# Optimization experiments

Hardware: AMD Instinct MI355X
Metric: run time of the kernel (lower is better)

Reference implementation:

```python
import jax, jax.numpy as jnp
import numpy as np

HEADS = 16
KV_HEADS = 8
HEAD_DIM = 128
HIDDEN = 2048
INTER = 8192
NUM_STATES = 4
WINDOW = 4096
EPS = 1e-6
THETA = 10000.0


def rms_norm(x, w):
    v = jnp.mean(jnp.square(x), axis=-1, keepdims=True)
    return x * jax.lax.rsqrt(v + EPS) * w


def rotate_half(x):
    h = x.shape[-1] // 2
    return jnp.concatenate((-x[..., h:], x[..., :h]), axis=-1)


def setup_inputs() -> dict:
    key = jax.random.key(0)
    ks = jax.random.split(key, 12)
    b, s = 1, 2048
    init = lambda k, shape: jax.random.normal(k, shape, jnp.float32) * 0.02
    return {
        "hidden_states": jax.random.normal(ks[0], (b, s, HIDDEN), jnp.float32),
        "sid": jax.random.randint(ks[1], (b, s), 0, NUM_STATES, dtype=jnp.int32),
        "position_ids": jnp.broadcast_to(jnp.arange(s, dtype=jnp.int32)[None, :], (b, s)),
        "ln1_w": jnp.ones((HIDDEN,), jnp.float32),
        "w_q": init(ks[2], (HEADS * HEAD_DIM, HIDDEN)),
        "w_k": init(ks[3], (KV_HEADS * HEAD_DIM, HIDDEN)),
        "w_v": init(ks[4], (KV_HEADS * HEAD_DIM, HIDDEN)),
        "w_o": init(ks[5], (HIDDEN, HEADS * HEAD_DIM)),
        "ln2_w": jnp.ones((HIDDEN,), jnp.float32),
        "w_gate": init(ks[6], (INTER, HIDDEN)),
        "w_up": init(ks[7], (INTER, HIDDEN)),
        "w_down": init(ks[8], (HIDDEN, INTER)),
    }


def reference(hidden_states, sid, position_ids, ln1_w, w_q, w_k, w_v, w_o, ln2_w, w_gate, w_up, w_down):
    b, s, _ = hidden_states.shape
    resid = hidden_states
    x = rms_norm(hidden_states, ln1_w)
    q = (x @ w_q.T).reshape(b, s, HEADS, HEAD_DIM).transpose(0, 2, 1, 3)      # [b,h,s,d]
    k = (x @ w_k.T).reshape(b, s, KV_HEADS, HEAD_DIM).transpose(0, 2, 1, 3)
    v = (x @ w_v.T).reshape(b, s, KV_HEADS, HEAD_DIM).transpose(0, 2, 1, 3)
    # RoPE (BoSsRotaryEmbedding + apply_rotary_pos_emb with unsqueeze_dim=1)
    inv_freq = 1.0 / (THETA ** (jnp.arange(0, HEAD_DIM, 2, dtype=jnp.float32) / HEAD_DIM))
    freqs = position_ids.astype(jnp.float32)[:, :, None] * inv_freq[None, None, :]  # [b,s,d/2]
    emb = jnp.concatenate((freqs, freqs), axis=-1)
    cos = jnp.cos(emb)[:, None]  # [b,1,s,d]
    sin = jnp.sin(emb)[:, None]
    q = q * cos + rotate_half(q) * sin
    k = k * cos + rotate_half(k) * sin
    # GQA: repeat_kv
    rep = HEADS // KV_HEADS
    k = jnp.repeat(k, rep, axis=1)
    v = jnp.repeat(v, rep, axis=1)
    # State-segment mask: stable sort by sid + causal varlen flash attention with
    # sliding window == dense attention masked to same-sid, causal, rank-window.
    same = sid[:, :, None] == sid[:, None, :]                                  # [b,s,s]
    causal = jnp.tril(jnp.ones((s, s), bool))
    tri = jnp.tril(jnp.ones((s, s), jnp.int32), -1)
    rank = jnp.einsum('bij,ij->bi', same.astype(jnp.int32), tri)               # within-segment position
    win = (rank[:, :, None] - rank[:, None, :]) <= WINDOW
    mask = same & causal[None] & win                                           # [b,s,s]
    scale = HEAD_DIM ** -0.5
    scores = jnp.einsum('bhqd,bhkd->bhqk', q, k) * scale
    scores = jnp.where(mask[:, None], scores, -jnp.inf)
    probs = jax.nn.softmax(scores, axis=-1)
    o = jnp.einsum('bhqk,bhkd->bhqd', probs, v)
    o = o.transpose(0, 2, 1, 3).reshape(b, s, HEADS * HEAD_DIM)
    h = resid + o @ w_o.T
    y = rms_norm(h, ln2_w)
    mlp = (jax.nn.silu(y @ w_gate.T) * (y @ w_up.T)) @ w_down.T
    return h + mlp
```

## Files before the change

### kernel.cpp

```cpp
#include <hip/hip_runtime.h>
#include <hip/hip_bf16.h>
#include <math.h>

#define SEQ    2048
#define HIDDEN 2048
#define INTER  8192
#define NHEADS 16
#define KVH    8
#define HD     128

typedef __bf16 bf16x8 __attribute__((ext_vector_type(8)));
typedef __bf16 bf16x4 __attribute__((ext_vector_type(4)));
typedef float  f32x4  __attribute__((ext_vector_type(4)));

typedef __attribute__((address_space(1))) void* as1v;
typedef __attribute__((address_space(3))) void* as3v;

__device__ __forceinline__ void g2l16(const void* g, void* l) {
    __builtin_amdgcn_global_load_lds((as1v)g, (as3v)l, 16, 0, 0);
}

#define OFF_WQ 0UL
#define OFF_WK 4194304UL
#define OFF_WV 6291456UL
#define OFF_WO 8388608UL
#define OFF_WG 12582912UL
#define OFF_WU 29360128UL
#define OFF_WD 46137344UL
#define W_TOTAL 62914560UL

__global__ __launch_bounds__(256) void k_cvt(
        const float* __restrict__ wq, const float* __restrict__ wk,
        const float* __restrict__ wv, const float* __restrict__ wo,
        const float* __restrict__ wg, const float* __restrict__ wu,
        const float* __restrict__ wd, __bf16* __restrict__ wb) {
    size_t e = ((size_t)blockIdx.x * 256 + threadIdx.x) * 8;
    const float* src; size_t base;
    if      (e < OFF_WK) { src = wq; base = OFF_WQ; }
    else if (e < OFF_WV) { src = wk; base = OFF_WK; }
    else if (e < OFF_WO) { src = wv; base = OFF_WV; }
    else if (e < OFF_WG) { src = wo; base = OFF_WO; }
    else if (e < OFF_WU) { src = wg; base = OFF_WG; }
    else if (e < OFF_WD) { src = wu; base = OFF_WU; }
    else                 { src = wd; base = OFF_WD; }
    const float4* s = (const float4*)(src + (e - base));
    float4 a = s[0], b = s[1];
    bf16x8 o;
    o[0] = (__bf16)a.x; o[1] = (__bf16)a.y; o[2] = (__bf16)a.z; o[3] = (__bf16)a.w;
    o[4] = (__bf16)b.x; o[5] = (__bf16)b.y; o[6] = (__bf16)b.z; o[7] = (__bf16)b.w;
    *(bf16x8*)(wb + e) = o;
}

__global__ __launch_bounds__(256) void k_rmsnorm(const float* __restrict__ x,
                                                 const float* __restrict__ w,
                                                 __bf16* __restrict__ out) {
    int row = blockIdx.x;
    int t   = threadIdx.x;
    const float4* xr = (const float4*)(x + (size_t)row * HIDDEN);
    float4 a = xr[t];
    float4 b = xr[t + 256];
    float ss = a.x*a.x + a.y*a.y + a.z*a.z + a.w*a.w
             + b.x*b.x + b.y*b.y + b.z*b.z + b.w*b.w;
#pragma unroll
    for (int d = 32; d > 0; d >>= 1) ss += __shfl_xor(ss, d);
    __shared__ float red[4];
    if ((t & 63) == 0) red[t >> 6] = ss;
    __syncthreads();
    float tot = red[0] + red[1] + red[2] + red[3];
    float r = rsqrtf(tot * (1.0f / (float)HIDDEN) + 1e-6f);
    const float4* wr = (const float4*)w;
    float4 wa = wr[t], wb = wr[t + 256];
    __bf16* o = out + (size_t)row * HIDDEN;
    bf16x4 pa, pb;
    pa[0] = (__bf16)(a.x * r * wa.x);
    pa[1] = (__bf16)(a.y * r * wa.y);
    pa[2] = (__bf16)(a.z * r * wa.z);
    pa[3] = (__bf16)(a.w * r * wa.w);
    pb[0] = (__bf16)(b.x * r * wb.x);
    pb[1] = (__bf16)(b.y * r * wb.y);
    pb[2] = (__bf16)(b.z * r * wb.z);
    pb[3] = (__bf16)(b.w * r * wb.w);
    *(bf16x4*)(o + 4*t)        = pa;
    *(bf16x4*)(o + 4*t + 1024) = pb;
}

__device__ __forceinline__ int gncol(int wn, int nt, int l15) {
    return wn*32 + ((nt & 1) << 4) + ((nt >> 1) << 6) + l15;
}

__device__ __forceinline__ void gemm_core(const __bf16* __restrict__ A, int lda,
                                          const __bf16* __restrict__ B, int ldb,
                                          int K, int m0, int n0,
                                          __bf16* As, __bf16* Bs,
                                          f32x4 acc[4][4]) {
    int tid  = threadIdx.x;
    int wave = tid >> 6;
    int lane = tid & 63;
    int quad = lane >> 4;
    int l15  = lane & 15;
    int wm = wave >> 1, wn = wave & 1;

    int srow = wave*32 + (lane >> 2);
    int scol = (lane & 3) * 8;
    char* adst = (char*)As + wave*2048 + lane*16;
    char* bdst = (char*)Bs + wave*2048 + lane*16;

    for (int k0 = 0; k0 < K; k0 += 32) {
        __syncthreads();
        g2l16(A + (size_t)(m0 + srow)      * lda + k0 + scol, adst);
        g2l16(A + (size_t)(m0 + srow + 16) * lda + k0 + scol, adst + 1024);
        g2l16(B + (size_t)(n0 + srow)      * ldb + k0 + scol, bdst);
        g2l16(B + (size_t)(n0 + srow + 16) * ldb + k0 + scol, bdst + 1024);
        __syncthreads();

        bf16x8 af[4], bfr[4];
#pragma unroll
        for (int mt = 0; mt < 4; ++mt)
            af[mt] = *(const bf16x8*)((const char*)As +
                        (wm*64 + mt*16 + l15)*64 + quad*16);
#pragma unroll
        for (int nt = 0; nt < 4; ++nt) {
            int r = gncol(wn, nt, l15);
            bfr[nt] = *(const bf16x8*)((const char*)Bs + r*64 + quad*16);
        }
#pragma unroll
        for (int mt = 0; mt < 4; ++mt)
#pragma unroll
            for (int nt = 0; nt < 4; ++nt)
                acc[mt][nt] = __builtin_amdgcn_mfma_f32_16x16x32_bf16(
                                  af[mt], bfr[nt], acc[mt][nt], 0, 0, 0);
    }
}

__device__ __forceinline__ void zero_acc(f32x4 acc[4][4]) {
#pragma unroll
    for (int i = 0; i < 4; ++i)
#pragma unroll
        for (int j = 0; j < 4; ++j) {
            acc[i][j][0] = 0.f; acc[i][j][1] = 0.f;
            acc[i][j][2] = 0.f; acc[i][j][3] = 0.f;
        }
}

#define MFMA_BF16 __builtin_amdgcn_mfma_f32_16x16x32_bf16
#define VMC asm volatile("s_waitcnt vmcnt(4)" ::: "memory")
#define NOSTMT ((void)0)

#define STAGE_A(BUF, HALF, TILE) do {                                         \
    const __bf16* _s = Aptr + (size_t)(m0 + (HALF)*128 + stgRow) * 2048       \
                      + ((size_t)(TILE) << 6) + stgCol;                       \
    char* _d = (char*)smem + (BUF)*65536 + (HALF)*16384 + stgDst;             \
    g2l16(_s, _d);                                                            \
    g2l16(_s + 8*2048, _d + 1024);                                            \
} while (0)

#define STAGE_B(BUF, HALF, TILE) do {                                         \
    const __bf16* _s = Bptr + (size_t)(n0 + (HALF)*128 + stgRow) * 2048       \
                      + ((size_t)(TILE) << 6) + stgCol;                       \
    char* _d = (char*)smem + (BUF)*65536 + 32768 + (HALF)*16384 + stgDst;     \
    g2l16(_s, _d);                                                            \
    g2l16(_s + 8*2048, _d + 1024);                                            \
} while (0)

#define PHASE(BUF, MH, NH, STAGE_STMT, VMWAIT) do {                           \
    bf16x8 _af[4][2], _bf[2][2];                                              \
    {                                                                         \
        const char* _Ab = (const char*)smem + (BUF)*65536 + (MH)*16384 + aRow;\
        const char* _Bb = (const char*)smem + (BUF)*65536 + 32768             \
                          + (NH)*16384 + bRow;                                \
        _Pragma("unroll")                                                     \
        for (int _m = 0; _m < 4; ++_m) {                                      \
            _af[_m][0] = *(const bf16x8*)(_Ab + _m*2048 + off0);              \
            _af[_m][1] = *(const bf16x8*)(_Ab + _m*2048 + (off0^64));         \
        }                                                                     \
        _Pragma("unroll")                                                     \
        for (int _n = 0; _n < 2; ++_n) {                                      \
            _bf[_n][0] = *(const bf16x8*)(_Bb + _n*2048 + off0);              \
            _bf[_n][1] = *(const bf16x8*)(_Bb + _n*2048 + (off0^64));         \
        }                                                                     \
    }                                                                         \
    STAGE_STMT;                                                               \
    VMWAIT;                                                                   \
    asm volatile("" ::: "memory");                                            \
    __builtin_amdgcn_s_barrier();                                             \
    asm volatile("" ::: "memory");                                            \
    __builtin_amdgcn_s_setprio(1);                                            \
    _Pragma("unroll")                                                         \
    for (int _m = 0; _m < 4; ++_m)                                            \
        _Pragma("unroll")                                                     \
        for (int _n = 0; _n < 2; ++_n) {                                      \
            acc[MH][NH][_m][_n] = MFMA_BF16(_af[_m][0], _bf[_n][0],           \
                                            acc[MH][NH][_m][_n], 0, 0, 0);    \
            acc[MH][NH][_m][_n] = MFMA_BF16(_af[_m][1], _bf[_n][1],           \
                                            acc[MH][NH][_m][_n], 0, 0, 0);    \
        }                                                                     \
    __builtin_amdgcn_s_setprio(0);                                            \
    asm volatile("" ::: "memory");                                            \
    __builtin_amdgcn_s_barrier();                                             \
    asm volatile("" ::: "memory");                                            \
} while (0)

__global__ __launch_bounds__(512, 2) void k_mlp256(
        const __bf16* __restrict__ Aptr,
        const __bf16* __restrict__ Bptr,
        __bf16* __restrict__ outb,
        int mode) {
    __shared__ char smem[131072];

    int flat = blockIdx.y * 32 + blockIdx.x;
    int swz  = (flat & 7) * 32 + (flat >> 3);
    int m0 = (swz >> 5) * 256;
    int n0 = (swz & 31) * 256;

    int tid  = threadIdx.x;
    int wave = tid >> 6, lane = tid & 63;
    int wm = wave >> 2, wn = wave & 3;
    int quad = lane >> 4, l15 = lane & 15;
    int cx   = l15 & 7;
    int off0 = (quad ^ cx) << 4;
    int aRow = (wm*64 + l15) << 7;
    int bRow = (wn*32 + l15) << 7;
    int stgRow = wave*16 + (lane >> 3);
    int stgCol = ((lane & 7) ^ (lane >> 3)) << 3;
    int stgDst = wave*2048 + lane*16;

    f32x4 acc[2][2][4][2];
#pragma unroll
    for (int a = 0; a < 2; ++a)
#pragma unroll
        for (int b = 0; b < 2; ++b)
#pragma unroll
            for (int c = 0; c < 4; ++c)
#pragma unroll
                for (int d = 0; d < 2; ++d) {
                    acc[a][b][c][d][0] = 0.f; acc[a][b][c][d][1] = 0.f;
                    acc[a][b][c][d][2] = 0.f; acc[a][b][c][d][3] = 0.f;
                }

    STAGE_A(0, 0, 0); STAGE_B(0, 0, 0);
    STAGE_A(0, 1, 0); STAGE_B(0, 1, 0);
    STAGE_A(1, 0, 1); STAGE_B(1, 0, 1);
    VMC;
    asm volatile("" ::: "memory");
    __builtin_amdgcn_s_barrier();
    asm volatile("" ::: "memory");

    const int NT = 32, TM = 31;
    for (int i = 0; i < NT/2; ++i) {
        int t1 = (2*i + 1) & TM;
        int t2 = (2*i + 2) & TM;
        int t3 = (2*i + 3) & TM;
        PHASE(0, 0, 0, STAGE_A(1, 1, t1), NOSTMT);
        PHASE(0, 0, 1, STAGE_B(1, 1, t1), NOSTMT);
        PHASE(0, 1, 0, STAGE_A(0, 0, t2), NOSTMT);
        PHASE(0, 1, 1, STAGE_B(0, 0, t2), VMC);
        PHASE(1, 0, 0, STAGE_A(0, 1, t2), NOSTMT);
        PHASE(1, 0, 1, STAGE_B(0, 1, t2), NOSTMT);
        PHASE(1, 1, 0, STAGE_A(1, 0, t3), NOSTMT);
        PHASE(1, 1, 1, STAGE_B(1, 0, t3), VMC);
    }

    int gm0 = m0 + wm*64 + quad*4;
    int gn0 = n0 + wn*32 + l15;
    if (mode == 0) {
#pragma unroll
        for (int mh = 0; mh < 2; ++mh)
#pragma unroll
            for (int nh = 0; nh < 2; ++nh)
#pragma unroll
                for (int mt2 = 0; mt2 < 4; ++mt2)
#pragma unroll
                    for (int nt2 = 0; nt2 < 2; ++nt2)
#pragma unroll
                        for (int r = 0; r < 4; ++r) {
                            int gm = gm0 + mh*128 + mt2*16 + r;
                            int gn = gn0 + nh*128 + nt2*16;
                            outb[(size_t)gm*INTER + gn] =
                                (__bf16)acc[mh][nh][mt2][nt2][r];
                        }
    } else {
#pragma unroll
        for (int mh = 0; mh < 2; ++mh)
#pragma unroll
            for (int nh = 0; nh < 2; ++nh)
#pragma unroll
                for (int mt2 = 0; mt2 < 4; ++mt2)
#pragma unroll
                    for (int nt2 = 0; nt2 < 2; ++nt2)
#pragma unroll
                        for (int r = 0; r < 4; ++r) {
                            int gm = gm0 + mh*128 + mt2*16 + r;
                            int gn = gn0 + nh*128 + nt2*16;
                            size_t idx = (size_t)gm*INTER + gn;
                            float g = acc[mh][nh][mt2][nt2][r];
                            float u = (float)outb[idx];
                            float s = g / (1.0f + __expf(-g));
                            outb[idx] = (__bf16)(s * u);
                        }
    }
}

__global__ __launch_bounds__(256) void k_gemm_qkv(
        const __bf16* __restrict__ x, const __bf16* __restrict__ wb,
        const int* __restrict__ pos_ids,
        __bf16* __restrict__ qb, __bf16* __restrict__ kb,
        __bf16* __restrict__ vtb) {
    __shared__ __bf16 As[128*32];
    __shared__ __bf16 Bs[128*32];
    int bn = blockIdx.x;
    int m0 = blockIdx.y * 128;
    const __bf16* B; int n0; int kind;
    if (bn < 16)      { B = wb + OFF_WQ; n0 = bn*128;      kind = 0; }
    else if (bn < 24) { B = wb + OFF_WK; n0 = (bn-16)*128; kind = 1; }
    else              { B = wb + OFF_WV; n0 = (bn-24)*128; kind = 2; }
    f32x4 acc[4][4]; zero_acc(acc);
    gemm_core(x, HIDDEN, B, HIDDEN, HIDDEN, m0, n0, As, Bs, acc);

    int tid = threadIdx.x, wave = tid >> 6, lane = tid & 63;
    int quad = lane >> 4, l15 = lane & 15, wm = wave >> 1, wn = wave & 1;

    if (kind == 2) {
#pragma unroll
        for (int mt = 0; mt < 4; ++mt)
#pragma unroll
            for (int nt = 0; nt < 4; ++nt) {
                int f  = n0 + gncol(wn, nt, l15);
                int gm = m0 + wm*64 + mt*16 + quad*4;
                bf16x4 vv;
                vv[0] = (__bf16)acc[mt][nt][0];
                vv[1] = (__bf16)acc[mt][nt][1];
                vv[2] = (__bf16)acc[mt][nt][2];
                vv[3] = (__bf16)acc[mt][nt][3];
                *(bf16x4*)(vtb + (size_t)f*2048 + gm) = vv;
            }
    } else {
        __bf16* out = (kind == 0) ? qb : kb;
        int ldc     = (kind == 0) ? 2048 : 1024;
        float scale = (kind == 0) ? 0.08838834764831845f : 1.0f;
        int i0 = wn*32 + l15;
        const float LN1E4_64 = 0.14391156831212787f;
        float f0 = __expf(-LN1E4_64 * (float)i0);
        float f1 = __expf(-LN1E4_64 * (float)(i0 + 16));
#pragma unroll
        for (int mt = 0; mt < 4; ++mt)
#pragma unroll
            for (int r = 0; r < 4; ++r) {
                int gm = m0 + wm*64 + mt*16 + quad*4 + r;
                float pos = (float)pos_ids[gm];
                float s0, c0, s1, c1;
                __sincosf(pos * f0, &s0, &c0);
                __sincosf(pos * f1, &s1, &c1);
                float a0 = acc[mt][0][r], a1 = acc[mt][1][r];
                float a2 = acc[mt][2][r], a3 = acc[mt][3][r];
                size_t rowb = (size_t)gm * ldc + n0 + wn*32 + l15;
                out[rowb]      = (__bf16)((a0*c0 - a2*s0) * scale);
                out[rowb + 16] = (__bf16)((a1*c1 - a3*s1) * scale);
                out[rowb + 64] = (__bf16)((a2*c0 + a0*s0) * scale);
                out[rowb + 80] = (__bf16)((a3*c1 + a1*s1) * scale);
            }
    }
}

__global__ __launch_bounds__(256) void k_gemm_oproj(
        const __bf16* __restrict__ ob, const __bf16* __restrict__ wo,
        const float* __restrict__ resid, float* __restrict__ h) {
    __shared__ __bf16 As[128*32];
    __shared__ __bf16 Bs[128*32];
    int n0 = blockIdx.x * 128, m0 = blockIdx.y * 128;
    f32x4 acc[4][4]; zero_acc(acc);
    gemm_core(ob, HIDDEN, wo, HIDDEN, HIDDEN, m0, n0, As, Bs, acc);
    int lane = threadIdx.x & 63, wave = threadIdx.x >> 6;
    int quad = lane >> 4, l15 = lane & 15, wm = wave >> 1, wn = wave & 1;
#pragma unroll
    for (int mt = 0; mt < 4; ++mt)
#pragma unroll
        for (int nt = 0; nt < 4; ++nt)
#pragma unroll
            for (int r = 0; r < 4; ++r) {
                int gm = m0 + wm*64 + mt*16 + quad*4 + r;
                int gn = n0 + gncol(wn, nt, l15);
                size_t idx = (size_t)gm*HIDDEN + gn;
                h[idx] = acc[mt][nt][r] + resid[idx];
            }
}

__global__ __launch_bounds__(256) void k_gemm_down(
        const __bf16* __restrict__ act, const __bf16* __restrict__ wd,
        const float* __restrict__ h, float* __restrict__ out) {
    __shared__ __bf16 As[128*32];
    __shared__ __bf16 Bs[128*32];
    int n0 = blockIdx.x * 128, m0 = blockIdx.y * 128;
    f32x4 acc[4][4]; zero_acc(acc);
    gemm_core(act, INTER, wd, INTER, INTER, m0, n0, As, Bs, acc);
    int lane = threadIdx.x & 63, wave = threadIdx.x >> 6;
    int quad = lane >> 4, l15 = lane & 15, wm = wave >> 1, wn = wave & 1;
#pragma unroll
    for (int mt = 0; mt < 4; ++mt)
#pragma unroll
        for (int nt = 0; nt < 4; ++nt)
#pragma unroll
            for (int r = 0; r < 4; ++r) {
                int gm = m0 + wm*64 + mt*16 + quad*4 + r;
                int gn = n0 + gncol(wn, nt, l15);
                size_t idx = (size_t)gm*HIDDEN + gn;
                out[idx] = acc[mt][nt][r] + h[idx];
            }
}

__global__ __launch_bounds__(256) void k_attn(
        const __bf16* __restrict__ qb,
        const __bf16* __restrict__ kb,
        const __bf16* __restrict__ vt,
        const int* __restrict__ sid,
        __bf16* __restrict__ o) {
    __shared__ int    sid_lds[SEQ];
    __shared__ __bf16 Kt[64*128];
    __shared__ __bf16 Vt[128*64];
    __shared__ __bf16 Pl[4*1024];

    int qt = blockIdx.x;
    int h  = blockIdx.y;
    int hk = h >> 1;
    int tid = threadIdx.x, wave = tid >> 6, lane = tid & 63;
    int quad = lane >> 4, l15 = lane & 15;
    int q0 = qt * 64;
    int qrow_base = q0 + wave * 16;

    for (int i = tid; i < SEQ; i += 256) sid_lds[i] = sid[i];

    bf16x8 qfrag[4];
#pragma unroll
    for (int seg = 0; seg < 4; ++seg)
        qfrag[seg] = *(const bf16x8*)(qb + (size_t)(qrow_base + l15)*2048
                                         + h*128 + seg*32 + quad*8);
    __syncthreads();
    int sq[4];
#pragma unroll
    for (int r = 0; r < 4; ++r) sq[r] = sid_lds[qrow_base + quad*4 + r];

    float m_i[4], l_i[4];
    f32x4 oacc[8];
#pragma unroll
    for (int r = 0; r < 4; ++r) { m_i[r] = -INFINITY; l_i[r] = 0.f; }
#pragma unroll
    for (int n = 0; n < 8; ++n) {
        oacc[n][0] = 0.f; oacc[n][1] = 0.f; oacc[n][2] = 0.f; oacc[n][3] = 0.f;
    }

    for (int kt = 0; kt <= qt; ++kt) {
        int k0 = kt * 64;
        __syncthreads();
#pragma unroll
        for (int t2 = 0; t2 < 4; ++t2) {
            int c   = wave*4 + t2;
            int row = c*4 + (lane >> 4);
            g2l16(kb + (size_t)(k0 + row)*1024 + hk*128 + (lane & 15)*8,
                  (char*)Kt + c*1024 + lane*16);
        }
#pragma unroll
        for (int t2 = 0; t2 < 4; ++t2) {
            int c   = wave*4 + t2;
            int row = c*8 + (lane >> 3);
            g2l16(vt + (size_t)(hk*128 + row)*2048 + k0 + (lane & 7)*8,
                  (char*)Vt + c*1024 + lane*16);
        }
        __syncthreads();

        f32x4 sacc[4];
#pragma unroll
        for (int nt = 0; nt < 4; ++nt) {
            sacc[nt][0]=0.f; sacc[nt][1]=0.f; sacc[nt][2]=0.f; sacc[nt][3]=0.f;
        }
#pragma unroll
        for (int seg = 0; seg < 4; ++seg)
#pragma unroll
            for (int nt = 0; nt < 4; ++nt) {
                bf16x8 kfr = *(const bf16x8*)((const char*)Kt +
                               (nt*16 + l15)*256 + seg*64 + quad*16);
                sacc[nt] = __builtin_amdgcn_mfma_f32_16x16x32_bf16(
                               qfrag[seg], kfr, sacc[nt], 0, 0, 0);
            }

        int sk[4], kg[4];
#pragma unroll
        for (int nt = 0; nt < 4; ++nt) {
            kg[nt] = k0 + nt*16 + l15;
            sk[nt] = sid_lds[kg[nt]];
        }
        float p[4][4];
#pragma unroll
        for (int r = 0; r < 4; ++r) {
            int qg = qrow_base + quad*4 + r;
            float mx = -INFINITY;
#pragma unroll
            for (int nt = 0; nt < 4; ++nt) {
                bool valid = (kg[nt] <= qg) && (sk[nt] == sq[r]);
                float s = valid ? sacc[nt][r] : -INFINITY;
                p[nt][r] = s;
                mx = fmaxf(mx, s);
            }
            mx = fmaxf(mx, __shfl_xor(mx, 1));
            mx = fmaxf(mx, __shfl_xor(mx, 2));
            mx = fmaxf(mx, __shfl_xor(mx, 4));
            mx = fmaxf(mx, __shfl_xor(mx, 8));
            float mn = fmaxf(m_i[r], mx);
            float alpha = (mn == m_i[r]) ? 1.0f : __expf(m_i[r] - mn);
            float rs = 0.f;
#pragma unroll
            for (int nt = 0; nt < 4; ++nt) {
                float pv = (p[nt][r] == -INFINITY) ? 0.f : __expf(p[nt][r] - mn);
                p[nt][r] = pv;
                rs += pv;
            }
            rs += __shfl_xor(rs, 1);
            rs += __shfl_xor(rs, 2);
            rs += __shfl_xor(rs, 4);
            rs += __shfl_xor(rs, 8);
            l_i[r] = l_i[r] * alpha + rs;
            m_i[r] = mn;
#pragma unroll
            for (int n = 0; n < 8; ++n) oacc[n][r] *= alpha;
        }

#pragma unroll
        for (int nt = 0; nt < 4; ++nt)
#pragma unroll
            for (int r = 0; r < 4; ++r)
                Pl[wave*1024 + (quad*4 + r)*64 + nt*16 + l15] = (__bf16)p[nt][r];
        __syncthreads();

#pragma unroll
        for (int kc = 0; kc < 2; ++kc) {
            bf16x8 pfrag = *(const bf16x8*)((const char*)Pl + wave*2048 +
                             l15*128 + kc*64 + quad*16);
#pragma unroll
            for (int n = 0; n < 8; ++n) {
                bf16x8 vfr = *(const bf16x8*)((const char*)Vt +
                               (n*16 + l15)*128 + kc*64 + quad*16);
                oacc[n] = __builtin_amdgcn_mfma_f32_16x16x32_bf16(
                              pfrag, vfr, oacc[n], 0, 0, 0);
            }
        }
    }

#pragma unroll
    for (int r = 0; r < 4; ++r) {
        float inv = 1.0f / l_i[r];
        size_t base = (size_t)(qrow_base + quad*4 + r)*2048 + h*128 + l15;
#pragma unroll
        for (int n = 0; n < 8; ++n)
            o[base + n*16] = (__bf16)(oacc[n][r] * inv);
    }
}

extern "C" void kernel_launch(void* const* d_in, const int* in_sizes, int n_in,
                              void* d_out, int out_size, void* d_ws, size_t ws_size,
                              hipStream_t stream) {
    (void)in_sizes; (void)n_in; (void)out_size; (void)ws_size;
    const float* hidden = (const float*)d_in[0];
    const int*   sid    = (const int*)d_in[1];
    const int*   pos    = (const int*)d_in[2];
    const float* ln1    = (const float*)d_in[3];
    const float* wq     = (const float*)d_in[4];
    const float* wk     = (const float*)d_in[5];
    const float* wv     = (const float*)d_in[6];
    const float* wo     = (const float*)d_in[7];
    const float* ln2    = (const float*)d_in[8];
    const float* wg     = (const float*)d_in[9];
    const float* wu     = (const float*)d_in[10];
    const float* wd     = (const float*)d_in[11];
    float* out = (float*)d_out;
    char*  ws  = (char*)d_ws;

    __bf16* wb   = (__bf16*)(ws);
    __bf16* xb   = (__bf16*)(ws + (120UL << 20));
    __bf16* qb   = (__bf16*)(ws + (128UL << 20));
    __bf16* kb   = (__bf16*)(ws + (136UL << 20));
    __bf16* vtb  = (__bf16*)(ws + (140UL << 20));
    __bf16* ob   = (__bf16*)(ws + (120UL << 20));
    float*  hbuf = (float*) (ws + (128UL << 20));
    __bf16* yb   = (__bf16*)(ws + (120UL << 20));
    __bf16* actb = (__bf16*)(ws + (144UL << 20));

    k_cvt<<<30720, 256, 0, stream>>>(wq, wk, wv, wo, wg, wu, wd, wb);
    k_rmsnorm<<<SEQ, 256, 0, stream>>>(hidden, ln1, xb);
    k_gemm_qkv<<<dim3(32, 16), 256, 0, stream>>>(xb, wb, pos, qb, kb, vtb);
    k_attn<<<dim3(32, 16), 256, 0, stream>>>(qb, kb, vtb, sid, ob);
    k_gemm_oproj<<<dim3(16, 16), 256, 0, stream>>>(ob, wb + OFF_WO, hidden, hbuf);
    k_rmsnorm<<<SEQ, 256, 0, stream>>>(hbuf, ln2, yb);
    k_mlp256<<<dim3(32, 8), 512, 0, stream>>>(yb, wb + OFF_WU, actb, 0);
    k_mlp256<<<dim3(32, 8), 512, 0, stream>>>(yb, wb + OFF_WG, actb, 1);
    k_gemm_down<<<dim3(16, 16), 256, 0, stream>>>(actb, wb + OFF_WD, hbuf, out);
}
```

Measured before the change: 822.1 us.

## Split-K the down projection onto the 256-tile MFMA pipeline with a reduce pass

The down projection (K=8192) now runs on the 256x256 pipelined MFMA GEMM core, split four ways along K so it launches 256 blocks, each writing fp32 partials. A separate reduce kernel sums the four partials and adds the residual. The intent is to replace the slower 128-tile down GEMM with the faster pipelined core while keeping enough blocks to fill the GPU. The cost is 64 MB of extra fp32 partial traffic plus one more launch, and the path depends on the workspace being at least 240 MB.

```diff
diff --git a/kernel.cpp b/kernel.cpp
--- a/kernel.cpp
+++ b/kernel.cpp
@@ -147,19 +147,19 @@
 #define NOSTMT ((void)0)
 
 #define STAGE_A(BUF, HALF, TILE) do {                                         \
-    const __bf16* _s = Aptr + (size_t)(m0 + (HALF)*128 + stgRow) * 2048       \
+    const __bf16* _s = Ag + (size_t)(m0 + (HALF)*128 + stgRow) * ldA          \
                       + ((size_t)(TILE) << 6) + stgCol;                       \
     char* _d = (char*)smem + (BUF)*65536 + (HALF)*16384 + stgDst;             \
     g2l16(_s, _d);                                                            \
-    g2l16(_s + 8*2048, _d + 1024);                                            \
+    g2l16(_s + 8*ldA, _d + 1024);                                             \
 } while (0)
 
 #define STAGE_B(BUF, HALF, TILE) do {                                         \
-    const __bf16* _s = Bptr + (size_t)(n0 + (HALF)*128 + stgRow) * 2048       \
+    const __bf16* _s = Bg + (size_t)(n0 + (HALF)*128 + stgRow) * ldB          \
                       + ((size_t)(TILE) << 6) + stgCol;                       \
     char* _d = (char*)smem + (BUF)*65536 + 32768 + (HALF)*16384 + stgDst;     \
     g2l16(_s, _d);                                                            \
-    g2l16(_s + 8*2048, _d + 1024);                                            \
+    g2l16(_s + 8*ldB, _d + 1024);                                             \
 } while (0)
 
 #define PHASE(BUF, MH, NH, STAGE_STMT, VMWAIT) do {                           \
@@ -200,6 +200,53 @@
     asm volatile("" ::: "memory");                                            \
 } while (0)
 
+#define P256_PRE                                                              \
+    int tid  = threadIdx.x;                                                   \
+    int wave = tid >> 6, lane = tid & 63;                                     \
+    int wm = wave >> 2, wn = wave & 3;                                        \
+    int quad = lane >> 4, l15 = lane & 15;                                    \
+    int cx   = l15 & 7;                                                       \
+    int off0 = (quad ^ cx) << 4;                                              \
+    int aRow = (wm*64 + l15) << 7;                                            \
+    int bRow = (wn*32 + l15) << 7;                                            \
+    int stgRow = wave*16 + (lane >> 3);                                       \
+    int stgCol = ((lane & 7) ^ (lane >> 3)) << 3;                             \
+    int stgDst = wave*2048 + lane*16;                                         \
+    f32x4 acc[2][2][4][2];                                                    \
+    _Pragma("unroll")                                                         \
+    for (int _a = 0; _a < 2; ++_a)                                            \
+        _Pragma("unroll")                                                     \
+        for (int _b = 0; _b < 2; ++_b)                                        \
+            _Pragma("unroll")                                                 \
+            for (int _c = 0; _c < 4; ++_c)                                    \
+                _Pragma("unroll")                                             \
+                for (int _d = 0; _d < 2; ++_d) {                              \
+                    acc[_a][_b][_c][_d][0] = 0.f; acc[_a][_b][_c][_d][1] = 0.f;\
+                    acc[_a][_b][_c][_d][2] = 0.f; acc[_a][_b][_c][_d][3] = 0.f;\
+                }
+
+#define P256_LOOP(NT)                                                         \
+    STAGE_A(0, 0, 0); STAGE_B(0, 0, 0);                                       \
+    STAGE_A(0, 1, 0); STAGE_B(0, 1, 0);                                       \
+    STAGE_A(1, 0, 1); STAGE_B(1, 0, 1);                                       \
+    VMC;                                                                      \
+    asm volatile("" ::: "memory");                                            \
+    __builtin_amdgcn_s_barrier();                                             \
+    asm volatile("" ::: "memory");                                            \
+    for (int i = 0; i < (NT)/2; ++i) {                                        \
+        int t1 = (2*i + 1) & ((NT)-1);                                        \
+        int t2 = (2*i + 2) & ((NT)-1);                                        \
+        int t3 = (2*i + 3) & ((NT)-1);                                        \
+        PHASE(0, 0, 0, STAGE_A(1, 1, t1), NOSTMT);                            \
+        PHASE(0, 0, 1, STAGE_B(1, 1, t1), NOSTMT);                            \
+        PHASE(0, 1, 0, STAGE_A(0, 0, t2), NOSTMT);                            \
+        PHASE(0, 1, 1, STAGE_B(0, 0, t2), VMC);                               \
+        PHASE(1, 0, 0, STAGE_A(0, 1, t2), NOSTMT);                            \
+        PHASE(1, 0, 1, STAGE_B(0, 1, t2), NOSTMT);                            \
+        PHASE(1, 1, 0, STAGE_A(1, 0, t3), NOSTMT);                            \
+        PHASE(1, 1, 1, STAGE_B(1, 0, t3), VMC);                               \
+    }
+
 __global__ __launch_bounds__(512, 2) void k_mlp256(
         const __bf16* __restrict__ Aptr,
         const __bf16* __restrict__ Bptr,
@@ -211,54 +258,12 @@
     int swz  = (flat & 7) * 32 + (flat >> 3);
     int m0 = (swz >> 5) * 256;
     int n0 = (swz & 31) * 256;
-
-    int tid  = threadIdx.x;
-    int wave = tid >> 6, lane = tid & 63;
-    int wm = wave >> 2, wn = wave & 3;
-    int quad = lane >> 4, l15 = lane & 15;
-    int cx   = l15 & 7;
-    int off0 = (quad ^ cx) << 4;
-    int aRow = (wm*64 + l15) << 7;
-    int bRow = (wn*32 + l15) << 7;
-    int stgRow = wave*16 + (lane >> 3);
-    int stgCol = ((lane & 7) ^ (lane >> 3)) << 3;
-    int stgDst = wave*2048 + lane*16;
-
-    f32x4 acc[2][2][4][2];
-#pragma unroll
-    for (int a = 0; a < 2; ++a)
-#pragma unroll
-        for (int b = 0; b < 2; ++b)
-#pragma unroll
-            for (int c = 0; c < 4; ++c)
-#pragma unroll
-                for (int d = 0; d < 2; ++d) {
-                    acc[a][b][c][d][0] = 0.f; acc[a][b][c][d][1] = 0.f;
-                    acc[a][b][c][d][2] = 0.f; acc[a][b][c][d][3] = 0.f;
-                }
-
-    STAGE_A(0, 0, 0); STAGE_B(0, 0, 0);
-    STAGE_A(0, 1, 0); STAGE_B(0, 1, 0);
-    STAGE_A(1, 0, 1); STAGE_B(1, 0, 1);
-    VMC;
-    asm volatile("" ::: "memory");
-    __builtin_amdgcn_s_barrier();
-    asm volatile("" ::: "memory");
-
-    const int NT = 32, TM = 31;
-    for (int i = 0; i < NT/2; ++i) {
-        int t1 = (2*i + 1) & TM;
-        int t2 = (2*i + 2) & TM;
-        int t3 = (2*i + 3) & TM;
-        PHASE(0, 0, 0, STAGE_A(1, 1, t1), NOSTMT);
-        PHASE(0, 0, 1, STAGE_B(1, 1, t1), NOSTMT);
-        PHASE(0, 1, 0, STAGE_A(0, 0, t2), NOSTMT);
-        PHASE(0, 1, 1, STAGE_B(0, 0, t2), VMC);
-        PHASE(1, 0, 0, STAGE_A(0, 1, t2), NOSTMT);
-        PHASE(1, 0, 1, STAGE_B(0, 1, t2), NOSTMT);
-        PHASE(1, 1, 0, STAGE_A(1, 0, t3), NOSTMT);
-        PHASE(1, 1, 1, STAGE_B(1, 0, t3), VMC);
-    }
+    const __bf16* Ag = Aptr;
+    const __bf16* Bg = Bptr;
+    const int ldA = 2048, ldB = 2048;
+
+    P256_PRE;
+    P256_LOOP(32);
 
     int gm0 = m0 + wm*64 + quad*4;
     int gn0 = n0 + wn*32 + l15;
@@ -298,6 +303,60 @@
                             outb[idx] = (__bf16)(s * u);
                         }
     }
+}
+
+__global__ __launch_bounds__(512, 2) void k_dsplit256(
+        const __bf16* __restrict__ Aptr,
+        const __bf16* __restrict__ Bptr,
+        float* __restrict__ pbuf) {
+    __shared__ char smem[131072];
+
+    int flat = blockIdx.x;
+    int swz  = (flat & 7) * 32 + (flat >> 3);
+    int kz = swz >> 6;
+    int m0 = ((swz >> 3) & 7) * 256;
+    int n0 = (swz & 7) * 256;
+    const __bf16* Ag = Aptr + (size_t)kz * 2048;
+    const __bf16* Bg = Bptr + (size_t)kz * 2048;
+    const int ldA = 8192, ldB = 8192;
+
+    P256_PRE;
+    P256_LOOP(32);
+
+    float* pout = pbuf + (size_t)kz * 4194304;
+    int gm0 = m0 + wm*64 + quad*4;
+    int gn0 = n0 + wn*32 + l15;
+#pragma unroll
+    for (int mh = 0; mh < 2; ++mh)
+#pragma unroll
+        for (int nh = 0; nh < 2; ++nh)
+#pragma unroll
+            for (int mt2 = 0; mt2 < 4; ++mt2)
+#pragma unroll
+                for (int nt2 = 0; nt2 < 2; ++nt2)
+#pragma unroll
+                    for (int r = 0; r < 4; ++r) {
+                        int gm = gm0 + mh*128 + mt2*16 + r;
+                        int gn = gn0 + nh*128 + nt2*16;
+                        pout[(size_t)gm*HIDDEN + gn] = acc[mh][nh][mt2][nt2][r];
+                    }
+}
+
+__global__ __launch_bounds__(256) void k_down_reduce(
+        const float* __restrict__ p, const float* __restrict__ h,
+        float* __restrict__ out) {
+    size_t i = ((size_t)blockIdx.x * 256 + threadIdx.x) * 4;
+    float4 a = *(const float4*)(p + i);
+    float4 b = *(const float4*)(p + 4194304 + i);
+    float4 c = *(const float4*)(p + 8388608 + i);
+    float4 d = *(const float4*)(p + 12582912 + i);
+    float4 hh = *(const float4*)(h + i);
+    float4 o;
+    o.x = a.x + b.x + c.x + d.x + hh.x;
+    o.y = a.y + b.y + c.y + d.y + hh.y;
+    o.z = a.z + b.z + c.z + d.z + hh.z;
+    o.w = a.w + b.w + c.w + d.w + hh.w;
+    *(float4*)(out + i) = o;
 }
 
 __global__ __launch_bounds__(256) void k_gemm_qkv(
@@ -556,7 +615,7 @@
 extern "C" void kernel_launch(void* const* d_in, const int* in_sizes, int n_in,
                               void* d_out, int out_size, void* d_ws, size_t ws_size,
                               hipStream_t stream) {
-    (void)in_sizes; (void)n_in; (void)out_size; (void)ws_size;
+    (void)in_sizes; (void)n_in; (void)out_size;
     const float* hidden = (const float*)d_in[0];
     const int*   sid    = (const int*)d_in[1];
     const int*   pos    = (const int*)d_in[2];
@@ -581,6 +640,7 @@
     float*  hbuf = (float*) (ws + (128UL << 20));
     __bf16* yb   = (__bf16*)(ws + (120UL << 20));
     __bf16* actb = (__bf16*)(ws + (144UL << 20));
+    float*  pbuf = (float*) (ws + (176UL << 20));
 
     k_cvt<<<30720, 256, 0, stream>>>(wq, wk, wv, wo, wg, wu, wd, wb);
     k_rmsnorm<<<SEQ, 256, 0, stream>>>(hidden, ln1, xb);
@@ -590,5 +650,10 @@
     k_rmsnorm<<<SEQ, 256, 0, stream>>>(hbuf, ln2, yb);
     k_mlp256<<<dim3(32, 8), 512, 0, stream>>>(yb, wb + OFF_WU, actb, 0);
     k_mlp256<<<dim3(32, 8), 512, 0, stream>>>(yb, wb + OFF_WG, actb, 1);
-    k_gemm_down<<<dim3(16, 16), 256, 0, stream>>>(actb, wb + OFF_WD, hbuf, out);
-}
+    if (ws_size >= (240UL << 20)) {
+        k_dsplit256<<<256, 512, 0, stream>>>(actb, wb + OFF_WD, pbuf);
+        k_down_reduce<<<4096, 256, 0, stream>>>(pbuf, hbuf, out);
+    } else {
+        k_gemm_down<<<dim3(16, 16), 256, 0, stream>>>(actb, wb + OFF_WD, hbuf, out);
+    }
+}
```

New measurement: 753.1 us. -8.4%, faster.
